# Performance work log

Hardware: AMD Instinct MI355X
Metric: run time of the kernel (lower is better)

Reference implementation:

```python
import jax, jax.numpy as jnp
import numpy as np

K = 3; STRIDE = 1; PAD = 1; DIL = 1; KN = K * K * K  # num_pts = 27


def _trilinear_sample(vol, grid):
    """F.grid_sample 3D, mode=bilinear, padding=zeros, align_corners=False.
    vol: (C, D, H, W); grid: (od, oh, ow, 3) with xyz order in [-1, 1].
    Returns (C, od, oh, ow)."""
    C, D, H, W = vol.shape
    # unnormalize (align_corners=False)
    ix = ((grid[..., 0] + 1.0) * W - 1.0) * 0.5
    iy = ((grid[..., 1] + 1.0) * H - 1.0) * 0.5
    iz = ((grid[..., 2] + 1.0) * D - 1.0) * 0.5
    x0 = jnp.floor(ix); y0 = jnp.floor(iy); z0 = jnp.floor(iz)
    out = jnp.zeros((C,) + grid.shape[:-1], vol.dtype)
    for dz in (0, 1):
        for dy in (0, 1):
            for dx in (0, 1):
                xc = x0 + dx; yc = y0 + dy; zc = z0 + dz
                w = (1.0 - jnp.abs(ix - xc)) * (1.0 - jnp.abs(iy - yc)) * (1.0 - jnp.abs(iz - zc))
                valid = (xc >= 0) & (xc < W) & (yc >= 0) & (yc < H) & (zc >= 0) & (zc < D)
                xi = jnp.clip(xc, 0, W - 1).astype(jnp.int32)
                yi = jnp.clip(yc, 0, H - 1).astype(jnp.int32)
                zi = jnp.clip(zc, 0, D - 1).astype(jnp.int32)
                val = vol[:, zi, yi, xi]  # (C, od, oh, ow)
                out = out + val * (w * valid.astype(vol.dtype))[None]
    return out


def setup_inputs() -> dict:
    key = jax.random.key(0)
    k1, k2, k3 = jax.random.split(key, 3)
    N, C, D, H, W = 2, 64, 16, 32, 32
    inp = jax.random.normal(k1, (N, C, D, H, W), dtype=jnp.float32)
    offset = jax.random.normal(k2, (N, KN * 3, D, H, W), dtype=jnp.float32)
    weight = jax.random.normal(k3, (64, 64, KN), dtype=jnp.float32) * 0.05
    return {"input": inp, "offset": offset, "weight": weight}


def reference(input, offset, weight):
    N, C, D, H, W = input.shape
    od, oh, ow = offset.shape[2], offset.shape[3], offset.shape[4]
    f32 = input.dtype
    # base sampling mesh (align_corners=True style normalization, as original)
    z = (jnp.arange(od) * STRIDE - PAD + ((K - 1) // 2) * DIL).astype(f32)
    y = (jnp.arange(oh) * STRIDE - PAD + ((K - 1) // 2) * DIL).astype(f32)
    x = (jnp.arange(ow) * STRIDE - PAD + ((K - 1) // 2) * DIL).astype(f32)
    mz, my, mx = jnp.meshgrid(z, y, x, indexing="ij")
    norm = lambda v, S: (v - (S - 1) / 2.0) / ((S - 1) / 2.0)
    mesh = jnp.stack([norm(mx, W), norm(my, H), norm(mz, D)], axis=-1)  # (od,oh,ow,3)
    # offsets: channel layout per kernel point is (dz, dy, dx)
    off = offset.reshape(N, KN, 3, od, oh, ow)
    goff = jnp.stack([
        off[:, :, 2] / ((W - 1) / 2.0),
        off[:, :, 1] / ((H - 1) / 2.0),
        off[:, :, 0] / ((D - 1) / 2.0),
    ], axis=-1)  # (N, KN, od, oh, ow, 3) xyz
    grid = mesh[None, None] + goff
    # per-batch, per-kernel-point trilinear gather -> (N, KN, C, od, oh, ow)
    sampled = jax.vmap(lambda v, g: jax.vmap(lambda gg: _trilinear_sample(v, gg))(g))(input, grid)
    # grouped matmul: weight (O, C, KN) flattened C-major matches sampled layout
    out = jnp.einsum("ock,nkcdhw->nodhw", weight, sampled)
    return out
```

## Files before the change

kernel.cpp:

```cpp
#include <hip/hip_runtime.h>

typedef __attribute__((ext_vector_type(8))) _Float16 half8;
typedef __attribute__((ext_vector_type(4))) float floatx4;

constexpr int NB  = 2;
constexpr int CC  = 64;
constexpr int DD  = 16;
constexpr int HH  = 32;
constexpr int WW  = 32;
constexpr int KN_ = 27;
constexpr int OC  = 64;
constexpr int DHW = DD * HH * WW;
constexpr int TP  = 16;
constexpr int KCH = 9;

__device__ __forceinline__ unsigned short f2h(float f) {
    _Float16 h = (_Float16)f;
    return *(unsigned short*)&h;
}

__global__ __launch_bounds__(256) void k_prep(const float* __restrict__ in,
                                              const float* __restrict__ w,
                                              unsigned int* __restrict__ outu,
                                              unsigned short* __restrict__ wf) {
    int bid = blockIdx.x;
    int t = threadIdx.x;
    if (bid < 512) {
        __shared__ float tile[64][65];
        int n  = bid >> 8;
        int v0 = (bid & 255) << 6;
        int lane = t & 63, row = t >> 6;
#pragma unroll
        for (int i = 0; i < 16; ++i) {
            int c = (i << 2) + row;
            tile[c][lane] = in[(size_t)(n * CC + c) * DHW + v0 + lane];
        }
        __syncthreads();
#pragma unroll
        for (int i = 0; i < 8; ++i) {
            int flat = i * 256 + t;
            int v = flat >> 5, cd = flat & 31;
            unsigned int lo = f2h(tile[2 * cd][v]);
            unsigned int hi = f2h(tile[2 * cd + 1][v]);
            outu[(size_t)(n * DHW + v0 + v) * 32 + cd] = lo | (hi << 16);
        }
    } else {
        int f = (bid - 512) * 256 + t;
        int i  = f & 7;
        int l  = (f >> 3) & 63;
        int ot = (f >> 9) & 3;
        int cc = (f >> 11) & 1;
        int k  = f >> 12;
        int o = ot * 16 + (l & 15);
        int c = cc * 32 + ((l >> 4) << 3) + i;
        wf[f] = f2h(w[(o * CC + c) * KN_ + k]);
    }
}

__global__ __launch_bounds__(128, 6) void k_main(const unsigned short* __restrict__ inp,
                                                 const unsigned short* __restrict__ wf,
                                                 const float* __restrict__ offs,
                                                 float* __restrict__ out) {
    __shared__ unsigned short S[2 * TP * 64];
    __shared__ unsigned int   SU[KCH * TP * 12];

    int t   = threadIdx.x;
    int bid = blockIdx.x;
    int n   = (bid >> 2) & 1;
    int idx = ((bid >> 3) << 2) | (bid & 3);
    int p0  = idx << 4;

    int sp = t >> 3;
    int cg = t & 7;
    int wv = t >> 6, l = t & 63;
    int lrow = l & 15, lk = l >> 4;

    const float* offb = offs + (size_t)n * (3 * KN_) * DHW + p0;
    const char*  inb  = (const char*)(inp + ((size_t)n * DHW << 6));

    floatx4 acc0 = {0.f, 0.f, 0.f, 0.f};
    floatx4 acc1 = {0.f, 0.f, 0.f, 0.f};

    const int cgo   = cg << 4;
    const int woff  = sp * 64 + ((cg ^ (sp & 7)) << 3);
    const int roff0 = lrow * 64 + (((0 | lk) ^ (lrow & 7)) << 3);
    const int roff1 = lrow * 64 + (((4 | lk) ^ (lrow & 7)) << 3);

    for (int ch = 0; ch < 3; ++ch) {
        __syncthreads();

        for (int si = t; si < KCH * TP; si += 128) {
            int kk = si >> 4, p = si & 15;
            int k  = ch * KCH + kk;
            int pa = p0 + p;
            int dpos = pa >> 10, hpos = (pa >> 5) & 31, wpos = pa & 31;

            float oz = offb[(k * 3 + 0) * DHW + p];
            float oy = offb[(k * 3 + 1) * DHW + p];
            float ox = offb[(k * 3 + 2) * DHW + p];
            float ix = ((float)wpos + ox) * (32.0f / 31.0f) - 0.5f;
            float iy = ((float)hpos + oy) * (32.0f / 31.0f) - 0.5f;
            float iz = ((float)dpos + oz) * (16.0f / 15.0f) - 0.5f;
            float xf = floorf(ix), yf = floorf(iy), zf = floorf(iz);
            float fx = ix - xf, fy = iy - yf, fz = iz - zf;
            int x0 = (int)xf, y0 = (int)yf, z0 = (int)zf;

            float wx0 = ((unsigned)x0       < (unsigned)WW) ? 1.f - fx : 0.f;
            float wx1 = ((unsigned)(x0 + 1) < (unsigned)WW) ? fx       : 0.f;
            float wy0 = ((unsigned)y0       < (unsigned)HH) ? 1.f - fy : 0.f;
            float wy1 = ((unsigned)(y0 + 1) < (unsigned)HH) ? fy       : 0.f;
            float wz0 = ((unsigned)z0       < (unsigned)DD) ? 1.f - fz : 0.f;
            float wz1 = ((unsigned)(z0 + 1) < (unsigned)DD) ? fz       : 0.f;

            int xc0 = min(max(x0, 0), WW - 1), xc1 = min(max(x0 + 1, 0), WW - 1);
            int yc0 = min(max(y0, 0), HH - 1), yc1 = min(max(y0 + 1, 0), HH - 1);
            int zc0 = min(max(z0, 0), DD - 1), zc1 = min(max(z0 + 1, 0), DD - 1);

            float wzy00 = wz0 * wy0, wzy01 = wz0 * wy1, wzy10 = wz1 * wy0, wzy11 = wz1 * wy1;
            unsigned int b00 = (zc0 * HH + yc0) * WW, b01 = (zc0 * HH + yc1) * WW;
            unsigned int b10 = (zc1 * HH + yc0) * WW, b11 = (zc1 * HH + yc1) * WW;

            uint4 vp, wp;
            vp.x = (b00 + xc0) | ((b00 + xc1) << 16);
            vp.y = (b01 + xc0) | ((b01 + xc1) << 16);
            vp.z = (b10 + xc0) | ((b10 + xc1) << 16);
            vp.w = (b11 + xc0) | ((b11 + xc1) << 16);
            wp.x = (unsigned int)f2h(wzy00 * wx0) | ((unsigned int)f2h(wzy00 * wx1) << 16);
            wp.y = (unsigned int)f2h(wzy01 * wx0) | ((unsigned int)f2h(wzy01 * wx1) << 16);
            wp.z = (unsigned int)f2h(wzy10 * wx0) | ((unsigned int)f2h(wzy10 * wx1) << 16);
            wp.w = (unsigned int)f2h(wzy11 * wx0) | ((unsigned int)f2h(wzy11 * wx1) << 16);

            unsigned int* rec = SU + si * 12;
            *(uint4*)rec       = vp;
            *(uint4*)(rec + 4) = wp;
        }
        __syncthreads();

        for (int kk = 0; kk < KCH; ++kk) {
            int k = ch * KCH + kk;

            const half8 wa00 = *(const half8*)(wf + ((((k << 1) | 0) * 4 + (wv << 1) + 0) << 9) + (l << 3));
            const half8 wa01 = *(const half8*)(wf + ((((k << 1) | 1) * 4 + (wv << 1) + 0) << 9) + (l << 3));
            const half8 wa10 = *(const half8*)(wf + ((((k << 1) | 0) * 4 + (wv << 1) + 1) << 9) + (l << 3));
            const half8 wa11 = *(const half8*)(wf + ((((k << 1) | 1) * 4 + (wv << 1) + 1) << 9) + (l << 3));

            const unsigned int* rec = SU + (kk * TP + sp) * 12;
            const uint4 vp = *(const uint4*)rec;
            const uint4 wp = *(const uint4*)(rec + 4);
            const unsigned int vpa[4] = {vp.x, vp.y, vp.z, vp.w};
            const unsigned int wpa[4] = {wp.x, wp.y, wp.z, wp.w};

            half8 accv = {0, 0, 0, 0, 0, 0, 0, 0};
#pragma unroll
            for (int cr = 0; cr < 8; ++cr) {
                unsigned int vd = vpa[cr >> 1];
                unsigned int wd = wpa[cr >> 1];
                unsigned int voxb = ((cr & 1) ? (vd >> 16) : (vd & 0xffffu)) << 7;
                unsigned short wu = (cr & 1) ? (unsigned short)(wd >> 16) : (unsigned short)wd;
                _Float16 wh = *(_Float16*)&wu;
                const half8 v = *(const half8*)(inb + voxb + cgo);
                half8 w8 = {wh, wh, wh, wh, wh, wh, wh, wh};
                accv += v * w8;
            }
            *(half8*)(S + ((k & 1) << 10) + woff) = accv;

            __syncthreads();

            const unsigned short* Sb = S + ((k & 1) << 10);
            const half8 bf0 = *(const half8*)(Sb + roff0);
            const half8 bf1 = *(const half8*)(Sb + roff1);
            acc0 = __builtin_amdgcn_mfma_f32_16x16x32_f16(wa00, bf0, acc0, 0, 0, 0);
            acc0 = __builtin_amdgcn_mfma_f32_16x16x32_f16(wa01, bf1, acc0, 0, 0, 0);
            acc1 = __builtin_amdgcn_mfma_f32_16x16x32_f16(wa10, bf0, acc1, 0, 0, 0);
            acc1 = __builtin_amdgcn_mfma_f32_16x16x32_f16(wa11, bf1, acc1, 0, 0, 0);
        }
    }

    float* ob = out + ((size_t)n * OC + (wv << 5) + (lk << 2)) * DHW + p0 + lrow;
#pragma unroll
    for (int r = 0; r < 4; ++r) {
        ob[r * DHW]              = acc0[r];
        ob[r * DHW + (DHW << 4)] = acc1[r];
    }
}

__global__ __launch_bounds__(256) void k_fallback(const float* __restrict__ inp,
                                                  const float* __restrict__ wt,
                                                  const float* __restrict__ offs,
                                                  float* __restrict__ out) {
    __shared__ float Slds[64][68];
    __shared__ float Wlds[64 * 64];
    int bid = blockIdx.x;
    int n = bid >> 8;
    int p0 = (bid & 255) * 64;
    int t = threadIdx.x;
    int cq = t & 15, c0 = cq << 2, pslot = t >> 4;
    int ob = (t & 15) << 2, pb = (t >> 4) << 2;
    int swz_w = (((cq & 7) ^ (cq >> 3)) << 2);
    float acc[4][4] = {};
    const float* offbase = offs + (size_t)n * (KN_ * 3) * DHW;
    for (int k = 0; k < KN_; ++k) {
#pragma unroll
        for (int i = 0; i < 16; ++i) {
            int f = i * 256 + t;
            int o = f & 63, c = f >> 6;
            Wlds[f] = wt[(o * CC + c) * KN_ + k];
        }
#pragma unroll
        for (int j = 0; j < 4; ++j) {
            int pl = pslot + 16 * j;
            int pa = p0 + pl;
            int d = pa >> 10, h = (pa >> 5) & 31, w = pa & 31;
            float offz = offbase[(k * 3 + 0) * DHW + pa];
            float offy = offbase[(k * 3 + 1) * DHW + pa];
            float offx = offbase[(k * 3 + 2) * DHW + pa];
            float ix = ((float)w + offx) * (32.0f / 31.0f) - 0.5f;
            float iy = ((float)h + offy) * (32.0f / 31.0f) - 0.5f;
            float iz = ((float)d + offz) * (16.0f / 15.0f) - 0.5f;
            float xf = floorf(ix), yf = floorf(iy), zf = floorf(iz);
            float fx = ix - xf, fy = iy - yf, fz = iz - zf;
            int x0 = (int)xf, y0 = (int)yf, z0 = (int)zf;
            float wx0 = 1.0f - fx, wx1 = fx, wy0 = 1.0f - fy, wy1 = fy, wz0 = 1.0f - fz, wz1 = fz;
            float s0 = 0.f, s1 = 0.f, s2 = 0.f, s3 = 0.f;
#pragma unroll
            for (int dz = 0; dz < 2; ++dz) {
                int zc = z0 + dz;
                if ((unsigned)zc >= (unsigned)DD) continue;
                float wz = dz ? wz1 : wz0;
#pragma unroll
                for (int dy = 0; dy < 2; ++dy) {
                    int yc = y0 + dy;
                    if ((unsigned)yc >= (unsigned)HH) continue;
                    float wzy = wz * (dy ? wy1 : wy0);
#pragma unroll
                    for (int dx = 0; dx < 2; ++dx) {
                        int xc = x0 + dx;
                        if ((unsigned)xc >= (unsigned)WW) continue;
                        float wf = wzy * (dx ? wx1 : wx0);
                        int vox = (zc * HH + yc) * WW + xc;
                        const float* b = inp + (size_t)(n * CC + c0) * DHW + vox;
                        s0 += wf * b[0]; s1 += wf * b[DHW];
                        s2 += wf * b[2 * DHW]; s3 += wf * b[3 * DHW];
                    }
                }
            }
            int plw = pl ^ swz_w;
            Slds[c0 + 0][plw] = s0; Slds[c0 + 1][plw] = s1;
            Slds[c0 + 2][plw] = s2; Slds[c0 + 3][plw] = s3;
        }
        __syncthreads();
#pragma unroll
        for (int c = 0; c < 64; ++c) {
            const int g = ((c >> 2) & 7) ^ (c >> 5);
            float4 wv = *(const float4*)(Wlds + c * 64 + ob);
            float4 sv = *(const float4*)(&Slds[c][pb ^ (g << 2)]);
            float wa[4] = {wv.x, wv.y, wv.z, wv.w};
            float sa[4] = {sv.x, sv.y, sv.z, sv.w};
#pragma unroll
            for (int i = 0; i < 4; ++i)
#pragma unroll
                for (int jj = 0; jj < 4; ++jj) acc[i][jj] += wa[i] * sa[jj];
        }
        __syncthreads();
    }
#pragma unroll
    for (int i = 0; i < 4; ++i) {
        float4 vv;
        vv.x = acc[i][0]; vv.y = acc[i][1]; vv.z = acc[i][2]; vv.w = acc[i][3];
        *(float4*)(out + (size_t)(n * OC + ob + i) * DHW + p0 + pb) = vv;
    }
}

extern "C" void kernel_launch(void* const* d_in, const int* in_sizes, int n_in,
                              void* d_out, int out_size, void* d_ws, size_t ws_size,
                              hipStream_t stream) {
    const float* inp = (const float*)d_in[0];
    const float* off = (const float*)d_in[1];
    const float* wgt = (const float*)d_in[2];
    float* out = (float*)d_out;

    const size_t in_f16_bytes = (size_t)NB * DHW * CC * 2;
    const size_t wf_bytes     = (size_t)KN_ * 2 * 4 * 64 * 8 * 2;

    if (ws_size >= in_f16_bytes + wf_bytes) {
        unsigned int*   in_t = (unsigned int*)d_ws;
        unsigned short* w_f  = (unsigned short*)((char*)d_ws + in_f16_bytes);
        k_prep<<<dim3(512 + 432), dim3(256), 0, stream>>>(inp, wgt, in_t, w_f);
        k_main<<<dim3(NB * 1024), dim3(128), 0, stream>>>(
            (const unsigned short*)in_t, w_f, off, out);
    } else {
        k_fallback<<<dim3(NB * 256), dim3(256), 0, stream>>>(inp, wgt, off, out);
    }
}
```

Before: 113.9 us.

## Double point tile per block, use 4 waves each owning 16 output channels

The main kernel now handles 32 spatial points per block with 256 threads and precomputes all 27 kernel points' sampling records in shared memory up front, instead of three chunks of 9. Each wave now owns 16 output channels across two 16-point column tiles, so each weight fragment loaded from global memory is reused for two MFMAs. The grid is halved, which trades fewer blocks and fewer chunk barriers for higher per-block LDS use and fewer resident waves.

Measured after the change: 109.7 us. 3.7% less time.

```diff
diff --git a/kernel.cpp b/kernel.cpp
--- a/kernel.cpp
+++ b/kernel.cpp
@@ -11,8 +11,7 @@
 constexpr int KN_ = 27;
 constexpr int OC  = 64;
 constexpr int DHW = DD * HH * WW;
-constexpr int TP  = 16;
-constexpr int KCH = 9;
+constexpr int TP  = 32;
 
 __device__ __forceinline__ unsigned short f2h(float f) {
     _Float16 h = (_Float16)f;
@@ -57,22 +56,24 @@
     }
 }
 
-__global__ __launch_bounds__(128, 6) void k_main(const unsigned short* __restrict__ inp,
+__global__ __launch_bounds__(256, 4) void k_main(const unsigned short* __restrict__ inp,
                                                  const unsigned short* __restrict__ wf,
                                                  const float* __restrict__ offs,
                                                  float* __restrict__ out) {
     __shared__ unsigned short S[2 * TP * 64];
-    __shared__ unsigned int   SU[KCH * TP * 12];
+    __shared__ uint4 SUV[KN_ * TP];
+    __shared__ uint4 SUW[KN_ * TP];
 
     int t   = threadIdx.x;
     int bid = blockIdx.x;
     int n   = (bid >> 2) & 1;
     int idx = ((bid >> 3) << 2) | (bid & 3);
-    int p0  = idx << 4;
+    int p0  = idx << 5;
 
     int sp = t >> 3;
     int cg = t & 7;
-    int wv = t >> 6, l = t & 63;
+    int w  = t >> 6;
+    int l  = t & 63;
     int lrow = l & 15, lk = l >> 4;
 
     const float* offb = offs + (size_t)n * (3 * KN_) * DHW + p0;
@@ -81,106 +82,101 @@
     floatx4 acc0 = {0.f, 0.f, 0.f, 0.f};
     floatx4 acc1 = {0.f, 0.f, 0.f, 0.f};
 
-    const int cgo   = cg << 4;
-    const int woff  = sp * 64 + ((cg ^ (sp & 7)) << 3);
-    const int roff0 = lrow * 64 + (((0 | lk) ^ (lrow & 7)) << 3);
-    const int roff1 = lrow * 64 + (((4 | lk) ^ (lrow & 7)) << 3);
-
-    for (int ch = 0; ch < 3; ++ch) {
-        __syncthreads();
-
-        for (int si = t; si < KCH * TP; si += 128) {
-            int kk = si >> 4, p = si & 15;
-            int k  = ch * KCH + kk;
-            int pa = p0 + p;
-            int dpos = pa >> 10, hpos = (pa >> 5) & 31, wpos = pa & 31;
-
-            float oz = offb[(k * 3 + 0) * DHW + p];
-            float oy = offb[(k * 3 + 1) * DHW + p];
-            float ox = offb[(k * 3 + 2) * DHW + p];
-            float ix = ((float)wpos + ox) * (32.0f / 31.0f) - 0.5f;
-            float iy = ((float)hpos + oy) * (32.0f / 31.0f) - 0.5f;
-            float iz = ((float)dpos + oz) * (16.0f / 15.0f) - 0.5f;
-            float xf = floorf(ix), yf = floorf(iy), zf = floorf(iz);
-            float fx = ix - xf, fy = iy - yf, fz = iz - zf;
-            int x0 = (int)xf, y0 = (int)yf, z0 = (int)zf;
-
-            float wx0 = ((unsigned)x0       < (unsigned)WW) ? 1.f - fx : 0.f;
-            float wx1 = ((unsigned)(x0 + 1) < (unsigned)WW) ? fx       : 0.f;
-            float wy0 = ((unsigned)y0       < (unsigned)HH) ? 1.f - fy : 0.f;
-            float wy1 = ((unsigned)(y0 + 1) < (unsigned)HH) ? fy       : 0.f;
-            float wz0 = ((unsigned)z0       < (unsigned)DD) ? 1.f - fz : 0.f;
-            float wz1 = ((unsigned)(z0 + 1) < (unsigned)DD) ? fz       : 0.f;
-
-            int xc0 = min(max(x0, 0), WW - 1), xc1 = min(max(x0 + 1, 0), WW - 1);
-            int yc0 = min(max(y0, 0), HH - 1), yc1 = min(max(y0 + 1, 0), HH - 1);
-            int zc0 = min(max(z0, 0), DD - 1), zc1 = min(max(z0 + 1, 0), DD - 1);
-
-            float wzy00 = wz0 * wy0, wzy01 = wz0 * wy1, wzy10 = wz1 * wy0, wzy11 = wz1 * wy1;
-            unsigned int b00 = (zc0 * HH + yc0) * WW, b01 = (zc0 * HH + yc1) * WW;
-            unsigned int b10 = (zc1 * HH + yc0) * WW, b11 = (zc1 * HH + yc1) * WW;
-
-            uint4 vp, wp;
-            vp.x = (b00 + xc0) | ((b00 + xc1) << 16);
-            vp.y = (b01 + xc0) | ((b01 + xc1) << 16);
-            vp.z = (b10 + xc0) | ((b10 + xc1) << 16);
-            vp.w = (b11 + xc0) | ((b11 + xc1) << 16);
-            wp.x = (unsigned int)f2h(wzy00 * wx0) | ((unsigned int)f2h(wzy00 * wx1) << 16);
-            wp.y = (unsigned int)f2h(wzy01 * wx0) | ((unsigned int)f2h(wzy01 * wx1) << 16);
-            wp.z = (unsigned int)f2h(wzy10 * wx0) | ((unsigned int)f2h(wzy10 * wx1) << 16);
-            wp.w = (unsigned int)f2h(wzy11 * wx0) | ((unsigned int)f2h(wzy11 * wx1) << 16);
-
-            unsigned int* rec = SU + si * 12;
-            *(uint4*)rec       = vp;
-            *(uint4*)(rec + 4) = wp;
-        }
-        __syncthreads();
-
-        for (int kk = 0; kk < KCH; ++kk) {
-            int k = ch * KCH + kk;
-
-            const half8 wa00 = *(const half8*)(wf + ((((k << 1) | 0) * 4 + (wv << 1) + 0) << 9) + (l << 3));
-            const half8 wa01 = *(const half8*)(wf + ((((k << 1) | 1) * 4 + (wv << 1) + 0) << 9) + (l << 3));
-            const half8 wa10 = *(const half8*)(wf + ((((k << 1) | 0) * 4 + (wv << 1) + 1) << 9) + (l << 3));
-            const half8 wa11 = *(const half8*)(wf + ((((k << 1) | 1) * 4 + (wv << 1) + 1) << 9) + (l << 3));
-
-            const unsigned int* rec = SU + (kk * TP + sp) * 12;
-            const uint4 vp = *(const uint4*)rec;
-            const uint4 wp = *(const uint4*)(rec + 4);
-            const unsigned int vpa[4] = {vp.x, vp.y, vp.z, vp.w};
-            const unsigned int wpa[4] = {wp.x, wp.y, wp.z, wp.w};
-
-            half8 accv = {0, 0, 0, 0, 0, 0, 0, 0};
-#pragma unroll
-            for (int cr = 0; cr < 8; ++cr) {
-                unsigned int vd = vpa[cr >> 1];
-                unsigned int wd = wpa[cr >> 1];
-                unsigned int voxb = ((cr & 1) ? (vd >> 16) : (vd & 0xffffu)) << 7;
-                unsigned short wu = (cr & 1) ? (unsigned short)(wd >> 16) : (unsigned short)wd;
-                _Float16 wh = *(_Float16*)&wu;
-                const half8 v = *(const half8*)(inb + voxb + cgo);
-                half8 w8 = {wh, wh, wh, wh, wh, wh, wh, wh};
-                accv += v * w8;
-            }
-            *(half8*)(S + ((k & 1) << 10) + woff) = accv;
-
-            __syncthreads();
-
-            const unsigned short* Sb = S + ((k & 1) << 10);
-            const half8 bf0 = *(const half8*)(Sb + roff0);
-            const half8 bf1 = *(const half8*)(Sb + roff1);
-            acc0 = __builtin_amdgcn_mfma_f32_16x16x32_f16(wa00, bf0, acc0, 0, 0, 0);
-            acc0 = __builtin_amdgcn_mfma_f32_16x16x32_f16(wa01, bf1, acc0, 0, 0, 0);
-            acc1 = __builtin_amdgcn_mfma_f32_16x16x32_f16(wa10, bf0, acc1, 0, 0, 0);
-            acc1 = __builtin_amdgcn_mfma_f32_16x16x32_f16(wa11, bf1, acc1, 0, 0, 0);
-        }
-    }
-
-    float* ob = out + ((size_t)n * OC + (wv << 5) + (lk << 2)) * DHW + p0 + lrow;
+    const int cgo  = cg << 4;
+    const int woff = sp * 64 + ((cg ^ (sp & 7)) << 3);
+    const int r0   = lrow;
+    const int r1   = 16 + lrow;
+    const int roff00 = r0 * 64 + (((0 | lk) ^ (r0 & 7)) << 3);
+    const int roff01 = r0 * 64 + (((4 | lk) ^ (r0 & 7)) << 3);
+    const int roff10 = r1 * 64 + (((0 | lk) ^ (r1 & 7)) << 3);
+    const int roff11 = r1 * 64 + (((4 | lk) ^ (r1 & 7)) << 3);
+
+    for (int si = t; si < KN_ * TP; si += 256) {
+        int k = si >> 5, p = si & 31;
+        int pa = p0 + p;
+        int dpos = pa >> 10, hpos = (pa >> 5) & 31, wpos = pa & 31;
+
+        float oz = offb[(k * 3 + 0) * DHW + p];
+        float oy = offb[(k * 3 + 1) * DHW + p];
+        float ox = offb[(k * 3 + 2) * DHW + p];
+        float ix = ((float)wpos + ox) * (32.0f / 31.0f) - 0.5f;
+        float iy = ((float)hpos + oy) * (32.0f / 31.0f) - 0.5f;
+        float iz = ((float)dpos + oz) * (16.0f / 15.0f) - 0.5f;
+        float xf = floorf(ix), yf = floorf(iy), zf = floorf(iz);
+        float fx = ix - xf, fy = iy - yf, fz = iz - zf;
+        int x0 = (int)xf, y0 = (int)yf, z0 = (int)zf;
+
+        float wx0 = ((unsigned)x0       < (unsigned)WW) ? 1.f - fx : 0.f;
+        float wx1 = ((unsigned)(x0 + 1) < (unsigned)WW) ? fx       : 0.f;
+        float wy0 = ((unsigned)y0       < (unsigned)HH) ? 1.f - fy : 0.f;
+        float wy1 = ((unsigned)(y0 + 1) < (unsigned)HH) ? fy       : 0.f;
+        float wz0 = ((unsigned)z0       < (unsigned)DD) ? 1.f - fz : 0.f;
+        float wz1 = ((unsigned)(z0 + 1) < (unsigned)DD) ? fz       : 0.f;
+
+        int xc0 = min(max(x0, 0), WW - 1), xc1 = min(max(x0 + 1, 0), WW - 1);
+        int yc0 = min(max(y0, 0), HH - 1), yc1 = min(max(y0 + 1, 0), HH - 1);
+        int zc0 = min(max(z0, 0), DD - 1), zc1 = min(max(z0 + 1, 0), DD - 1);
+
+        float wzy00 = wz0 * wy0, wzy01 = wz0 * wy1, wzy10 = wz1 * wy0, wzy11 = wz1 * wy1;
+        unsigned int b00 = (zc0 * HH + yc0) * WW, b01 = (zc0 * HH + yc1) * WW;
+        unsigned int b10 = (zc1 * HH + yc0) * WW, b11 = (zc1 * HH + yc1) * WW;
+
+        uint4 vp, wp;
+        vp.x = (b00 + xc0) | ((b00 + xc1) << 16);
+        vp.y = (b01 + xc0) | ((b01 + xc1) << 16);
+        vp.z = (b10 + xc0) | ((b10 + xc1) << 16);
+        vp.w = (b11 + xc0) | ((b11 + xc1) << 16);
+        wp.x = (unsigned int)f2h(wzy00 * wx0) | ((unsigned int)f2h(wzy00 * wx1) << 16);
+        wp.y = (unsigned int)f2h(wzy01 * wx0) | ((unsigned int)f2h(wzy01 * wx1) << 16);
+        wp.z = (unsigned int)f2h(wzy10 * wx0) | ((unsigned int)f2h(wzy10 * wx1) << 16);
+        wp.w = (unsigned int)f2h(wzy11 * wx0) | ((unsigned int)f2h(wzy11 * wx1) << 16);
+
+        SUV[si] = vp;
+        SUW[si] = wp;
+    }
+    __syncthreads();
+
+    for (int k = 0; k < KN_; ++k) {
+        const half8 wa0 = *(const half8*)(wf + (((((k << 1) | 0) << 2) + w) << 9) + (l << 3));
+        const half8 wa1 = *(const half8*)(wf + (((((k << 1) | 1) << 2) + w) << 9) + (l << 3));
+
+        const uint4 vp = SUV[(k << 5) + sp];
+        const uint4 wp = SUW[(k << 5) + sp];
+        const unsigned int vpa[4] = {vp.x, vp.y, vp.z, vp.w};
+        const unsigned int wpa[4] = {wp.x, wp.y, wp.z, wp.w};
+
+        half8 accv = {0, 0, 0, 0, 0, 0, 0, 0};
+#pragma unroll
+        for (int cr = 0; cr < 8; ++cr) {
+            unsigned int vd = vpa[cr >> 1];
+            unsigned int voxb = ((cr & 1) ? (vd >> 16) : (vd & 0xffffu)) << 7;
+            unsigned int wd = wpa[cr >> 1];
+            unsigned short wu = (cr & 1) ? (unsigned short)(wd >> 16) : (unsigned short)wd;
+            _Float16 wh = *(_Float16*)&wu;
+            const half8 v = *(const half8*)(inb + voxb + cgo);
+            half8 w8 = {wh, wh, wh, wh, wh, wh, wh, wh};
+            accv += v * w8;
+        }
+        *(half8*)(S + ((k & 1) << 11) + woff) = accv;
+
+        __syncthreads();
+
+        const unsigned short* Sb = S + ((k & 1) << 11);
+        const half8 bf00 = *(const half8*)(Sb + roff00);
+        const half8 bf01 = *(const half8*)(Sb + roff01);
+        const half8 bf10 = *(const half8*)(Sb + roff10);
+        const half8 bf11 = *(const half8*)(Sb + roff11);
+        acc0 = __builtin_amdgcn_mfma_f32_16x16x32_f16(wa0, bf00, acc0, 0, 0, 0);
+        acc0 = __builtin_amdgcn_mfma_f32_16x16x32_f16(wa1, bf01, acc0, 0, 0, 0);
+        acc1 = __builtin_amdgcn_mfma_f32_16x16x32_f16(wa0, bf10, acc1, 0, 0, 0);
+        acc1 = __builtin_amdgcn_mfma_f32_16x16x32_f16(wa1, bf11, acc1, 0, 0, 0);
+    }
+
+    float* ob = out + ((size_t)n * OC + (w << 4) + (lk << 2)) * DHW + p0 + lrow;
 #pragma unroll
     for (int r = 0; r < 4; ++r) {
-        ob[r * DHW]              = acc0[r];
-        ob[r * DHW + (DHW << 4)] = acc1[r];
+        ob[r * DHW]      = acc0[r];
+        ob[r * DHW + 16] = acc1[r];
     }
 }
 
@@ -286,7 +282,7 @@
         unsigned int*   in_t = (unsigned int*)d_ws;
         unsigned short* w_f  = (unsigned short*)((char*)d_ws + in_f16_bytes);
         k_prep<<<dim3(512 + 432), dim3(256), 0, stream>>>(inp, wgt, in_t, w_f);
-        k_main<<<dim3(NB * 1024), dim3(128), 0, stream>>>(
+        k_main<<<dim3(1024), dim3(256), 0, stream>>>(
             (const unsigned short*)in_t, w_f, off, out);
     } else {
         k_fallback<<<dim3(NB * 256), dim3(256), 0, stream>>>(inp, wgt, off, out);
```
